# Performance work log

Measured on AMD Instinct MI355X. Metric: run time of the kernel, lower is better.

## Reference

```python
import jax, jax.numpy as jnp
import numpy as np


def setup_inputs() -> dict:
    key = jax.random.key(0)
    k1, k2, k3 = jax.random.split(key, 3)
    B, S, I, H, M = 8, 2048, 256, 256, 1024
    x = jax.random.normal(k1, (B, S, I), dtype=jnp.float32)
    mem = jax.random.normal(k2, (B, M, H), dtype=jnp.float32)
    # Xavier-uniform with gain=sqrt(2): bound = sqrt(2)*sqrt(6/(H+I))
    bound = np.sqrt(2.0) * np.sqrt(6.0 / (H + I))
    W = jax.random.uniform(k3, (H, I), dtype=jnp.float32, minval=-bound, maxval=bound)
    return {"x": x, "mem": mem, "W": W}


def reference(x, mem, W):
    # key[b,s,h] = relu(sum_i x[b,s,i] * W[h,i])  -- one batched GEMM for all t
    key_seq = jax.nn.relu(jnp.einsum("bsi,hi->bsh", x, W))
    # val[b,s,m] = sum_h key[b,s,h] * mem[b,m,h]
    val_seq = jnp.einsum("bsh,bmh->bsm", key_seq, mem)
    return key_seq, val_seq
```

## Files before the change

kernel.cpp:

```cpp
#include <hip/hip_runtime.h>
#include <cstdint>

typedef unsigned short u16;
typedef __bf16 bf16x8 __attribute__((ext_vector_type(8)));
typedef float f32x4 __attribute__((ext_vector_type(4)));
typedef u16 u16x8 __attribute__((ext_vector_type(8)));

#define NX 4194304L

__device__ __forceinline__ u16 f2bf(float f) {
  union { float f; uint32_t u; } v; v.f = f;
  uint32_t r = v.u + 0x7fffu + ((v.u >> 16) & 1u);
  return (u16)(r >> 16);
}

__device__ __forceinline__ u16x8 cvt8(float4 a, float4 b) {
  u16x8 o;
  o[0]=f2bf(a.x); o[1]=f2bf(a.y); o[2]=f2bf(a.z); o[3]=f2bf(a.w);
  o[4]=f2bf(b.x); o[5]=f2bf(b.y); o[6]=f2bf(b.z); o[7]=f2bf(b.w);
  return o;
}

__device__ __forceinline__ int sw_addr(int row, int k) {
  return row * 256 + ((((k >> 3) ^ (row & 7)) << 3)) + (k & 7);
}

template<bool A_BF16, bool RELU, bool STORE_BF16>
__global__ __launch_bounds__(256, 2)
void gemm_direct(const void* __restrict__ Ap, const float* __restrict__ Bp,
                 float* __restrict__ C, u16* __restrict__ Cbf, int N,
                 long sA_batch, long sB_batch, long sC_batch)
{
  constexpr int K = 256;
  __shared__ __align__(16) u16 sB[128 * 256];

  const int tid  = threadIdx.x;
  const int wave = tid >> 6;
  const int lane = tid & 63;
  const int quad = lane >> 4;
  const int r    = lane & 15;
  const int wm   = wave >> 1;
  const int wn   = wave & 1;
  const int bm   = blockIdx.y * 128;
  const int bn   = blockIdx.x * 128;
  const int batch = blockIdx.z;

  {
    const int rowS = tid >> 1;
    const int colS = (tid & 1) * 16;
    const float* Bg = Bp + (long)batch * sB_batch + (long)(bn + rowS) * K + colS;
    #pragma unroll
    for (int c = 0; c < 8; ++c) {
      const float* p = Bg + c * 32;
      float4 f0 = *(const float4*)(p);
      float4 f1 = *(const float4*)(p + 4);
      float4 f2 = *(const float4*)(p + 8);
      float4 f3 = *(const float4*)(p + 12);
      u16x8 lo = cvt8(f0, f1);
      u16x8 hi = cvt8(f2, f3);
      const int col = colS + c * 32;
      *(u16x8*)(sB + sw_addr(rowS, col))     = lo;
      *(u16x8*)(sB + sw_addr(rowS, col + 8)) = hi;
    }
  }
  __syncthreads();

  const float* Af = nullptr;
  const u16*   Ah = nullptr;
  if (A_BF16) Ah = (const u16*)Ap   + (long)batch * sA_batch + (long)(bm + wm * 64 + r) * K;
  else        Af = (const float*)Ap + (long)batch * sA_batch + (long)(bm + wm * 64 + r) * K;

  f32x4 acc[4][4];
  #pragma unroll
  for (int i = 0; i < 4; i++)
    #pragma unroll
    for (int j = 0; j < 4; j++)
      acc[i][j] = f32x4{0.f, 0.f, 0.f, 0.f};

  #pragma unroll 2
  for (int kt = 0; kt < K; kt += 32) {
    bf16x8 af[4], bf[4];
    #pragma unroll
    for (int i = 0; i < 4; ++i) {
      if (A_BF16) {
        af[i] = *(const bf16x8*)(Ah + (long)i * 16 * K + kt + quad * 8);
      } else {
        const float* p = Af + (long)i * 16 * K + kt + quad * 8;
        float4 a0 = *(const float4*)(p);
        float4 a1 = *(const float4*)(p + 4);
        u16x8 t = cvt8(a0, a1);
        af[i] = *(bf16x8*)&t;
      }
    }
    #pragma unroll
    for (int j = 0; j < 4; ++j)
      bf[j] = *(const bf16x8*)(sB + sw_addr(wn * 64 + j * 16 + r, kt + quad * 8));
    #pragma unroll
    for (int i = 0; i < 4; ++i)
      #pragma unroll
      for (int j = 0; j < 4; ++j)
        acc[i][j] = __builtin_amdgcn_mfma_f32_16x16x32_bf16(af[i], bf[j], acc[i][j], 0, 0, 0);
  }

  float* Co = C + (long)batch * sC_batch;
  u16*   Bo = STORE_BF16 ? (Cbf + (long)batch * sC_batch) : nullptr;
  #pragma unroll
  for (int i = 0; i < 4; i++) {
    #pragma unroll
    for (int j = 0; j < 4; j++) {
      #pragma unroll
      for (int reg = 0; reg < 4; reg++) {
        const int row = bm + wm * 64 + i * 16 + quad * 4 + reg;
        const int col = bn + wn * 64 + j * 16 + r;
        float v = acc[i][j][reg];
        if (RELU) v = v > 0.f ? v : 0.f;
        const long idx = (long)row * N + col;
        Co[idx] = v;
        if (STORE_BF16) Bo[idx] = f2bf(v);
      }
    }
  }
}

extern "C" void kernel_launch(void* const* d_in, const int* in_sizes, int n_in,
                              void* d_out, int out_size, void* d_ws, size_t ws_size,
                              hipStream_t stream) {
  const float* x   = (const float*)d_in[0];
  const float* mem = (const float*)d_in[1];
  const float* W   = (const float*)d_in[2];
  float* out   = (float*)d_out;
  float* key_f = out;
  float* val_f = out + NX;
  u16* key_bf  = (u16*)d_ws;

  dim3 g1(2, 128, 1);
  gemm_direct<false, true, true><<<g1, 256, 0, stream>>>(
      (const void*)x, W, key_f, key_bf, 256, 0, 0, 0);

  dim3 g2(8, 16, 8);
  gemm_direct<true, false, false><<<g2, 256, 0, stream>>>(
      (const void*)key_bf, mem, val_f, nullptr, 1024,
      (long)2048 * 256, (long)1024 * 256, (long)2048 * 1024);
}
```

Baseline: 138.5 us.

## Drop bf16 key workspace, read fp32 key directly, add XCD-aware block mapping

The first GEMM no longer writes a bf16 copy of the key activations. The second GEMM now reads the fp32 key output and converts it to bf16 in registers. The second launch becomes a 1D grid whose low block-index bits select the batch, so blocks of one batch land on the same XCD and can share its L2 for mem and key. This saves the extra bf16 store but doubles the bytes read for the A operand in the second GEMM.

```diff
diff --git a/kernel.cpp b/kernel.cpp
--- a/kernel.cpp
+++ b/kernel.cpp
@@ -25,14 +25,25 @@
   return row * 256 + ((((k >> 3) ^ (row & 7)) << 3)) + (k & 7);
 }
 
-template<bool A_BF16, bool RELU, bool STORE_BF16>
+template<bool RELU, bool XCD_MAP>
 __global__ __launch_bounds__(256, 2)
-void gemm_direct(const void* __restrict__ Ap, const float* __restrict__ Bp,
-                 float* __restrict__ C, u16* __restrict__ Cbf, int N,
+void gemm_direct(const float* __restrict__ Ap, const float* __restrict__ Bp,
+                 float* __restrict__ C, int N,
                  long sA_batch, long sB_batch, long sC_batch)
 {
   constexpr int K = 256;
   __shared__ __align__(16) u16 sB[128 * 256];
+
+  int bm, bn, batch;
+  if (XCD_MAP) {
+    const int bid = blockIdx.x;
+    batch = bid & 7;
+    const int t = bid >> 3;
+    bm = (t & 15) * 128;
+    bn = (t >> 4) * 128;
+  } else {
+    bn = blockIdx.x * 128; bm = blockIdx.y * 128; batch = 0;
+  }
 
   const int tid  = threadIdx.x;
   const int wave = tid >> 6;
@@ -41,9 +52,6 @@
   const int r    = lane & 15;
   const int wm   = wave >> 1;
   const int wn   = wave & 1;
-  const int bm   = blockIdx.y * 128;
-  const int bn   = blockIdx.x * 128;
-  const int batch = blockIdx.z;
 
   {
     const int rowS = tid >> 1;
@@ -65,10 +73,7 @@
   }
   __syncthreads();
 
-  const float* Af = nullptr;
-  const u16*   Ah = nullptr;
-  if (A_BF16) Ah = (const u16*)Ap   + (long)batch * sA_batch + (long)(bm + wm * 64 + r) * K;
-  else        Af = (const float*)Ap + (long)batch * sA_batch + (long)(bm + wm * 64 + r) * K;
+  const float* Af = Ap + (long)batch * sA_batch + (long)(bm + wm * 64 + r) * K;
 
   f32x4 acc[4][4];
   #pragma unroll
@@ -82,15 +87,11 @@
     bf16x8 af[4], bf[4];
     #pragma unroll
     for (int i = 0; i < 4; ++i) {
-      if (A_BF16) {
-        af[i] = *(const bf16x8*)(Ah + (long)i * 16 * K + kt + quad * 8);
-      } else {
-        const float* p = Af + (long)i * 16 * K + kt + quad * 8;
-        float4 a0 = *(const float4*)(p);
-        float4 a1 = *(const float4*)(p + 4);
-        u16x8 t = cvt8(a0, a1);
-        af[i] = *(bf16x8*)&t;
-      }
+      const float* p = Af + (long)i * 16 * K + kt + quad * 8;
+      float4 a0 = *(const float4*)(p);
+      float4 a1 = *(const float4*)(p + 4);
+      u16x8 t = cvt8(a0, a1);
+      af[i] = *(bf16x8*)&t;
     }
     #pragma unroll
     for (int j = 0; j < 4; ++j)
@@ -103,7 +104,6 @@
   }
 
   float* Co = C + (long)batch * sC_batch;
-  u16*   Bo = STORE_BF16 ? (Cbf + (long)batch * sC_batch) : nullptr;
   #pragma unroll
   for (int i = 0; i < 4; i++) {
     #pragma unroll
@@ -114,9 +114,7 @@
         const int col = bn + wn * 64 + j * 16 + r;
         float v = acc[i][j][reg];
         if (RELU) v = v > 0.f ? v : 0.f;
-        const long idx = (long)row * N + col;
-        Co[idx] = v;
-        if (STORE_BF16) Bo[idx] = f2bf(v);
+        Co[(long)row * N + col] = v;
       }
     }
   }
@@ -131,14 +129,13 @@
   float* out   = (float*)d_out;
   float* key_f = out;
   float* val_f = out + NX;
-  u16* key_bf  = (u16*)d_ws;
+  (void)d_ws; (void)ws_size;
 
   dim3 g1(2, 128, 1);
-  gemm_direct<false, true, true><<<g1, 256, 0, stream>>>(
-      (const void*)x, W, key_f, key_bf, 256, 0, 0, 0);
+  gemm_direct<true, false><<<g1, 256, 0, stream>>>(
+      x, W, key_f, 256, 0, 0, 0);
 
-  dim3 g2(8, 16, 8);
-  gemm_direct<true, false, false><<<g2, 256, 0, stream>>>(
-      (const void*)key_bf, mem, val_f, nullptr, 1024,
+  gemm_direct<false, true><<<dim3(1024, 1, 1), 256, 0, stream>>>(
+      key_f, mem, val_f, 1024,
       (long)2048 * 256, (long)1024 * 256, (long)2048 * 1024);
 }
```

New measurement: 149.0 us. +7.6%, slower.

## Stage GEMM tiles via global_load_lds and pre-convert mem to bf16 in first kernel

Applied to the files above, without the earlier changes.

Both GEMMs now stream K-slices of A and B into LDS with direct global-to-LDS loads. The first GEMM stages fp32 tiles with an XOR swizzle and converts to bf16 when reading from LDS. The first kernel also converts mem to bf16 into workspace, so the second GEMM reads bf16 B instead of converting fp32 per block. This removes uncoalesced per-lane global A reads and the repeated B conversion. In exchange it adds two barriers per K-step with no double buffering, and an extra pass over mem.

```diff
diff --git a/kernel.cpp b/kernel.cpp
--- a/kernel.cpp
+++ b/kernel.cpp
@@ -6,7 +6,8 @@
 typedef float f32x4 __attribute__((ext_vector_type(4)));
 typedef u16 u16x8 __attribute__((ext_vector_type(8)));
 
-#define NX 4194304L
+#define NX   4194304L
+#define NMEM 2097152L
 
 __device__ __forceinline__ u16 f2bf(float f) {
   union { float f; uint32_t u; } v; v.f = f;
@@ -21,19 +22,114 @@
   return o;
 }
 
-__device__ __forceinline__ int sw_addr(int row, int k) {
-  return row * 256 + ((((k >> 3) ^ (row & 7)) << 3)) + (k & 7);
-}
-
-template<bool A_BF16, bool RELU, bool STORE_BF16>
 __global__ __launch_bounds__(256, 2)
-void gemm_direct(const void* __restrict__ Ap, const float* __restrict__ Bp,
-                 float* __restrict__ C, u16* __restrict__ Cbf, int N,
-                 long sA_batch, long sB_batch, long sC_batch)
+void gemm1_kernel(const float* __restrict__ x, const float* __restrict__ W,
+                  float* __restrict__ key_f, u16* __restrict__ key_bf,
+                  const float* __restrict__ mem, u16* __restrict__ mem_bf)
 {
   constexpr int K = 256;
-  __shared__ __align__(16) u16 sB[128 * 256];
-
+  __shared__ __align__(16) float sA[128 * 32];
+  __shared__ __align__(16) float sB[128 * 32];
+
+  const int tid  = threadIdx.x;
+  const int wave = tid >> 6;
+  const int lane = tid & 63;
+  const int quad = lane >> 4;
+  const int r    = lane & 15;
+  const int wm   = wave >> 1;
+  const int wn   = wave & 1;
+  const int bm   = blockIdx.y * 128;
+  const int bn   = blockIdx.x * 128;
+
+  const int o_base = wave * 1024 + lane * 16;
+
+  f32x4 acc[4][4];
+  #pragma unroll
+  for (int i = 0; i < 4; i++)
+    #pragma unroll
+    for (int j = 0; j < 4; j++)
+      acc[i][j] = f32x4{0.f, 0.f, 0.f, 0.f};
+
+  for (int kt = 0; kt < K; kt += 32) {
+    __syncthreads();
+    #pragma unroll
+    for (int rr = 0; rr < 4; rr++) {
+      const int o   = rr * 4096 + o_base;
+      const int row = o >> 7;
+      const int cp  = (o >> 4) & 7;
+      const int c   = cp ^ (row & 7);
+      const char* ga = (const char*)x + (long)(bm + row) * 1024 + kt * 4 + c * 16;
+      const char* gb = (const char*)W + (long)(bn + row) * 1024 + kt * 4 + c * 16;
+      char* la = (char*)sA + rr * 4096 + wave * 1024;
+      char* lb = (char*)sB + rr * 4096 + wave * 1024;
+      __builtin_amdgcn_global_load_lds((const __attribute__((address_space(1))) void*)ga,
+                                       (__attribute__((address_space(3))) void*)la, 16, 0, 0);
+      __builtin_amdgcn_global_load_lds((const __attribute__((address_space(1))) void*)gb,
+                                       (__attribute__((address_space(3))) void*)lb, 16, 0, 0);
+    }
+    __syncthreads();
+
+    bf16x8 af[4], bfr[4];
+    const int s = r & 7;
+    #pragma unroll
+    for (int i = 0; i < 4; ++i) {
+      const float* base = sA + (wm * 64 + i * 16 + r) * 32;
+      float4 f0 = *(const float4*)(base + (((2 * quad)     ^ s) << 2));
+      float4 f1 = *(const float4*)(base + (((2 * quad + 1) ^ s) << 2));
+      u16x8 t = cvt8(f0, f1);
+      af[i] = *(bf16x8*)&t;
+    }
+    #pragma unroll
+    for (int j = 0; j < 4; ++j) {
+      const float* base = sB + (wn * 64 + j * 16 + r) * 32;
+      float4 f0 = *(const float4*)(base + (((2 * quad)     ^ s) << 2));
+      float4 f1 = *(const float4*)(base + (((2 * quad + 1) ^ s) << 2));
+      u16x8 t = cvt8(f0, f1);
+      bfr[j] = *(bf16x8*)&t;
+    }
+    #pragma unroll
+    for (int i = 0; i < 4; ++i)
+      #pragma unroll
+      for (int j = 0; j < 4; ++j)
+        acc[i][j] = __builtin_amdgcn_mfma_f32_16x16x32_bf16(af[i], bfr[j], acc[i][j], 0, 0, 0);
+  }
+
+  #pragma unroll
+  for (int i = 0; i < 4; i++) {
+    #pragma unroll
+    for (int j = 0; j < 4; j++) {
+      #pragma unroll
+      for (int reg = 0; reg < 4; reg++) {
+        const int row = bm + wm * 64 + i * 16 + quad * 4 + reg;
+        const int col = bn + wn * 64 + j * 16 + r;
+        float v = acc[i][j][reg];
+        v = v > 0.f ? v : 0.f;
+        const long idx = (long)row * 256 + col;
+        key_f[idx]  = v;
+        key_bf[idx] = f2bf(v);
+      }
+    }
+  }
+
+  {
+    const int bid = blockIdx.y * 2 + blockIdx.x;
+    const long e0 = ((long)bid * 256 + tid) * 32;
+    #pragma unroll
+    for (int c = 0; c < 4; ++c) {
+      float4 f0 = *(const float4*)(mem + e0 + c * 8);
+      float4 f1 = *(const float4*)(mem + e0 + c * 8 + 4);
+      *(u16x8*)(mem_bf + e0 + c * 8) = cvt8(f0, f1);
+    }
+  }
+}
+
+__global__ __launch_bounds__(256, 2)
+void gemm2_kernel(const u16* __restrict__ A, const u16* __restrict__ B,
+                  float* __restrict__ C)
+{
+  constexpr int K = 256;
+  __shared__ __align__(16) u16 sA[128 * 32];
+  __shared__ __align__(16) u16 sB[128 * 32];
   const int tid  = threadIdx.x;
   const int wave = tid >> 6;
   const int lane = tid & 63;
@@ -45,30 +141,9 @@
   const int bn   = blockIdx.x * 128;
   const int batch = blockIdx.z;
 
-  {
-    const int rowS = tid >> 1;
-    const int colS = (tid & 1) * 16;
-    const float* Bg = Bp + (long)batch * sB_batch + (long)(bn + rowS) * K + colS;
-    #pragma unroll
-    for (int c = 0; c < 8; ++c) {
-      const float* p = Bg + c * 32;
-      float4 f0 = *(const float4*)(p);
-      float4 f1 = *(const float4*)(p + 4);
-      float4 f2 = *(const float4*)(p + 8);
-      float4 f3 = *(const float4*)(p + 12);
-      u16x8 lo = cvt8(f0, f1);
-      u16x8 hi = cvt8(f2, f3);
-      const int col = colS + c * 32;
-      *(u16x8*)(sB + sw_addr(rowS, col))     = lo;
-      *(u16x8*)(sB + sw_addr(rowS, col + 8)) = hi;
-    }
-  }
-  __syncthreads();
-
-  const float* Af = nullptr;
-  const u16*   Ah = nullptr;
-  if (A_BF16) Ah = (const u16*)Ap   + (long)batch * sA_batch + (long)(bm + wm * 64 + r) * K;
-  else        Af = (const float*)Ap + (long)batch * sA_batch + (long)(bm + wm * 64 + r) * K;
+  const char* Ab = (const char*)(A + (long)batch * 2048 * 256);
+  const char* Bb = (const char*)(B + (long)batch * 1024 * 256);
+  const long ldr = 512;
 
   f32x4 acc[4][4];
   #pragma unroll
@@ -77,33 +152,41 @@
     for (int j = 0; j < 4; j++)
       acc[i][j] = f32x4{0.f, 0.f, 0.f, 0.f};
 
-  #pragma unroll 2
+  const int o0 = wave * 1024 + lane * 16;
+
   for (int kt = 0; kt < K; kt += 32) {
+    __syncthreads();
+    #pragma unroll
+    for (int rr = 0; rr < 2; rr++) {
+      const int o    = rr * 4096 + o0;
+      const int row  = o >> 6;
+      const int colb = o & 63;
+      const char* ga = Ab + (long)(bm + row) * ldr + (long)kt * 2 + colb;
+      const char* gb = Bb + (long)(bn + row) * ldr + (long)kt * 2 + colb;
+      char* la = (char*)sA + rr * 4096 + wave * 1024;
+      char* lb = (char*)sB + rr * 4096 + wave * 1024;
+      __builtin_amdgcn_global_load_lds((const __attribute__((address_space(1))) void*)ga,
+                                       (__attribute__((address_space(3))) void*)la, 16, 0, 0);
+      __builtin_amdgcn_global_load_lds((const __attribute__((address_space(1))) void*)gb,
+                                       (__attribute__((address_space(3))) void*)lb, 16, 0, 0);
+    }
+    __syncthreads();
+
     bf16x8 af[4], bf[4];
     #pragma unroll
-    for (int i = 0; i < 4; ++i) {
-      if (A_BF16) {
-        af[i] = *(const bf16x8*)(Ah + (long)i * 16 * K + kt + quad * 8);
-      } else {
-        const float* p = Af + (long)i * 16 * K + kt + quad * 8;
-        float4 a0 = *(const float4*)(p);
-        float4 a1 = *(const float4*)(p + 4);
-        u16x8 t = cvt8(a0, a1);
-        af[i] = *(bf16x8*)&t;
-      }
-    }
-    #pragma unroll
-    for (int j = 0; j < 4; ++j)
-      bf[j] = *(const bf16x8*)(sB + sw_addr(wn * 64 + j * 16 + r, kt + quad * 8));
-    #pragma unroll
-    for (int i = 0; i < 4; ++i)
-      #pragma unroll
-      for (int j = 0; j < 4; ++j)
+    for (int i = 0; i < 4; i++)
+      af[i] = *(const bf16x8*)(sA + (wm * 64 + i * 16 + r) * 32 + quad * 8);
+    #pragma unroll
+    for (int j = 0; j < 4; j++)
+      bf[j] = *(const bf16x8*)(sB + (wn * 64 + j * 16 + r) * 32 + quad * 8);
+    #pragma unroll
+    for (int i = 0; i < 4; i++)
+      #pragma unroll
+      for (int j = 0; j < 4; j++)
         acc[i][j] = __builtin_amdgcn_mfma_f32_16x16x32_bf16(af[i], bf[j], acc[i][j], 0, 0, 0);
   }
 
-  float* Co = C + (long)batch * sC_batch;
-  u16*   Bo = STORE_BF16 ? (Cbf + (long)batch * sC_batch) : nullptr;
+  float* Co = C + (long)batch * 2048 * 1024;
   #pragma unroll
   for (int i = 0; i < 4; i++) {
     #pragma unroll
@@ -112,11 +195,7 @@
       for (int reg = 0; reg < 4; reg++) {
         const int row = bm + wm * 64 + i * 16 + quad * 4 + reg;
         const int col = bn + wn * 64 + j * 16 + r;
-        float v = acc[i][j][reg];
-        if (RELU) v = v > 0.f ? v : 0.f;
-        const long idx = (long)row * N + col;
-        Co[idx] = v;
-        if (STORE_BF16) Bo[idx] = f2bf(v);
+        Co[(long)row * 1024 + col] = acc[i][j][reg];
       }
     }
   }
@@ -132,13 +211,11 @@
   float* key_f = out;
   float* val_f = out + NX;
   u16* key_bf  = (u16*)d_ws;
+  u16* mem_bf  = (u16*)d_ws + NX;
 
   dim3 g1(2, 128, 1);
-  gemm_direct<false, true, true><<<g1, 256, 0, stream>>>(
-      (const void*)x, W, key_f, key_bf, 256, 0, 0, 0);
+  gemm1_kernel<<<g1, 256, 0, stream>>>(x, W, key_f, key_bf, mem, mem_bf);
 
   dim3 g2(8, 16, 8);
-  gemm_direct<true, false, false><<<g2, 256, 0, stream>>>(
-      (const void*)key_bf, mem, val_f, nullptr, 1024,
-      (long)2048 * 256, (long)1024 * 256, (long)2048 * 1024);
-}
+  gemm2_kernel<<<g2, 256, 0, stream>>>(key_bf, mem_bf, val_f);
+}
```

New measurement: 129.2 us. 6.7% less time.
